# Performance work log

Measured on AMD Instinct MI355X. Metric: run time of the kernel, lower is better.

## Reference

```python
import jax, jax.numpy as jnp
import numpy as np
from jax import lax

STEPS = 200
LR = 0.01
BATCH = 16384
PROJ = 8
HID = 64


def setup_inputs() -> dict:
    key = jax.random.key(0)
    k_spec, k_w1, k_w2, k_r = jax.random.split(key, 4)
    spectrum = jax.random.normal(k_spec, (BATCH, 40), dtype=jnp.float32)
    # forward_model params: MLP 6 -> 64 (tanh) -> 40
    W1 = jax.random.normal(k_w1, (6, HID), dtype=jnp.float32) * 0.3
    b1 = jnp.zeros((HID,), dtype=jnp.float32)
    W2 = jax.random.normal(k_w2, (HID, 40), dtype=jnp.float32) * 0.3
    b2 = jnp.zeros((40,), dtype=jnp.float32)
    # random projection, row-normalized (as in __init__)
    R = jax.random.normal(k_r, (PROJ, 40), dtype=jnp.float32)
    R = R / jnp.linalg.norm(R, axis=1, keepdims=True)
    return {"spectrum": spectrum, "W1": W1, "b1": b1, "W2": W2, "b2": b2, "R": R}


def reference(spectrum, W1, b1, W2, b2, R):
    def fwd_model(u):  # (6,) -> (40,)
        return jnp.tanh(u @ W1 + b1) @ W2 + b2

    def solve(spec):  # spec: (40,) -> u: (6,)
        def step(u, _):
            g_pred = fwd_model(u)
            error = g_pred - spec               # (40,)
            z = R @ error                       # (PROJ,)
            grad_est = R.T @ z                  # (40,)
            u = u - LR * grad_est[:6]
            u = jnp.clip(u, 0.0, 1.0)           # clamp=True
            return u, None

        u0 = jnp.full((6,), 0.5, dtype=spec.dtype)
        u_final, _ = lax.scan(step, u0, None, length=STEPS)
        return u_final

    return jax.vmap(solve)(spectrum)  # (BATCH, 6)
```

## Files before the change

kernel.cpp:

```cpp
#include <hip/hip_runtime.h>


static constexpr float LR_ = 0.01f;

typedef float v2f __attribute__((ext_vector_type(2)));

__device__ __forceinline__ void pin2(v2f& x) { asm volatile("" : "+v"(x)); }

__global__ __launch_bounds__(256)
__attribute__((amdgpu_waves_per_eu(2, 2)))
void solve_k(
    const float* __restrict__ spec, const float* __restrict__ W1,
    const float* __restrict__ b1,   const float* __restrict__ W2,
    const float* __restrict__ b2,   const float* __restrict__ R,
    float* __restrict__ out, int batch)
{
    __shared__ float sQs[64 * 7];
    __shared__ float sSs[240];

    const int t = threadIdx.x;

    if (t < 64) {
        float M[8];
        #pragma unroll
        for (int p = 0; p < 8; ++p) {
            float acc = 0.f;
            for (int k = 0; k < 40; ++k) acc = fmaf(W2[t*40+k], R[p*40+k], acc);
            M[p] = acc;
        }
        #pragma unroll
        for (int j = 0; j < 6; ++j) {
            float acc = 0.f;
            #pragma unroll
            for (int p = 0; p < 8; ++p) acc = fmaf(M[p], R[p*40+j], acc);
            sQs[t*7+j] = -LR_ * acc;
        }
    } else {
        for (int idx = t - 64; idx < 240; idx += 192) {
            int j = idx / 40, k = idx % 40;
            float acc = 0.f;
            #pragma unroll
            for (int p = 0; p < 8; ++p) acc = fmaf(R[p*40+j], R[p*40+k], acc);
            sSs[idx] = -LR_ * acc;
        }
    }
    __syncthreads();

    const int tid = blockIdx.x * 256 + t;
    const int s   = tid >> 3;
    const int sub = tid & 7;
    const int ib  = sub * 8;
    const bool live = (s < batch);
    const int sl = live ? s : 0;

    const float K = 2.8853900817779268f;

    v2f w1kp[6][4], b1kp[4];
    #pragma unroll
    for (int j = 0; j < 6; ++j)
        #pragma unroll
        for (int ip = 0; ip < 4; ++ip) {
            w1kp[j][ip].x = K * W1[j*64 + ib + 2*ip];
            w1kp[j][ip].y = K * W1[j*64 + ib + 2*ip + 1];
        }
    #pragma unroll
    for (int ip = 0; ip < 4; ++ip) {
        b1kp[ip].x = K * b1[ib + 2*ip];
        b1kp[ip].y = K * b1[ib + 2*ip + 1];
    }

    v2f qs2p[8][3];
    float qc[6];
    #pragma unroll
    for (int j = 0; j < 6; ++j) qc[j] = 0.f;
    #pragma unroll
    for (int i = 0; i < 8; ++i)
        #pragma unroll
        for (int m = 0; m < 3; ++m) {
            float a = sQs[(ib + i)*7 + 2*m];
            float b = sQs[(ib + i)*7 + 2*m + 1];
            qs2p[i][m].x = -2.f * a;
            qs2p[i][m].y = -2.f * b;
            qc[2*m]   += a;
            qc[2*m+1] += b;
        }

    float es[6];
    #pragma unroll
    for (int j = 0; j < 6; ++j) es[j] = 0.f;
    const float* sp = spec + sl * 40;
    for (int k = 0; k < 40; ++k) {
        float v = b2[k] - sp[k];
        #pragma unroll
        for (int j = 0; j < 6; ++j) es[j] = fmaf(v, sSs[j*40+k], es[j]);
    }
    v2f c2[3];
    #pragma unroll
    for (int m = 0; m < 3; ++m) {
        c2[m].x = es[2*m]   * 0.125f + qc[2*m];
        c2[m].y = es[2*m+1] * 0.125f + qc[2*m+1];
    }

    #pragma unroll
    for (int j = 0; j < 6; ++j)
        #pragma unroll
        for (int ip = 0; ip < 4; ++ip) pin2(w1kp[j][ip]);
    #pragma unroll
    for (int ip = 0; ip < 4; ++ip) pin2(b1kp[ip]);
    #pragma unroll
    for (int i = 0; i < 8; ++i)
        #pragma unroll
        for (int m = 0; m < 3; ++m) pin2(qs2p[i][m]);
    #pragma unroll
    for (int m = 0; m < 3; ++m) pin2(c2[m]);

    float u[6];
    #pragma unroll
    for (int j = 0; j < 6; ++j) u[j] = 0.5f;

    for (int step = 0; step < 200; ++step) {
        float r[8];
        #pragma unroll
        for (int ip = 0; ip < 4; ++ip) {
            v2f tt = b1kp[ip];
            #pragma unroll
            for (int j = 0; j < 6; ++j) {
                v2f ub = {u[j], u[j]};
                tt = __builtin_elementwise_fma(ub, w1kp[j][ip], tt);
            }
            v2f e1;
            e1.x = __builtin_amdgcn_exp2f(tt.x);
            e1.y = __builtin_amdgcn_exp2f(tt.y);
            e1 += (v2f){1.f, 1.f};
            float rab = __builtin_amdgcn_rcpf(e1.x * e1.y);
            r[2*ip]   = e1.y * rab;
            r[2*ip+1] = e1.x * rab;
        }
        v2f g2[3];
        #pragma unroll
        for (int m = 0; m < 3; ++m) {
            v2f up = {u[2*m], u[2*m+1]};
            g2[m] = __builtin_elementwise_fma(up, (v2f){0.125f, 0.125f}, c2[m]);
        }
        #pragma unroll
        for (int i = 0; i < 8; ++i) {
            v2f hb = {r[i], r[i]};
            #pragma unroll
            for (int m = 0; m < 3; ++m)
                g2[m] = __builtin_elementwise_fma(hb, qs2p[i][m], g2[m]);
        }
        float a0 = g2[0].x, a1 = g2[0].y, a2 = g2[1].x,
              a3 = g2[1].y, a4 = g2[2].x, a5 = g2[2].y;
        asm("s_nop 1\n\t"
            "v_add_f32_dpp %0, %0, %0 quad_perm:[1,0,3,2] row_mask:0xf bank_mask:0xf bound_ctrl:0\n\t"
            "v_add_f32_dpp %1, %1, %1 quad_perm:[1,0,3,2] row_mask:0xf bank_mask:0xf bound_ctrl:0\n\t"
            "v_add_f32_dpp %2, %2, %2 quad_perm:[1,0,3,2] row_mask:0xf bank_mask:0xf bound_ctrl:0\n\t"
            "v_add_f32_dpp %3, %3, %3 quad_perm:[1,0,3,2] row_mask:0xf bank_mask:0xf bound_ctrl:0\n\t"
            "v_add_f32_dpp %4, %4, %4 quad_perm:[1,0,3,2] row_mask:0xf bank_mask:0xf bound_ctrl:0\n\t"
            "v_add_f32_dpp %5, %5, %5 quad_perm:[1,0,3,2] row_mask:0xf bank_mask:0xf bound_ctrl:0\n\t"
            "v_add_f32_dpp %0, %0, %0 quad_perm:[2,3,0,1] row_mask:0xf bank_mask:0xf bound_ctrl:0\n\t"
            "v_add_f32_dpp %1, %1, %1 quad_perm:[2,3,0,1] row_mask:0xf bank_mask:0xf bound_ctrl:0\n\t"
            "v_add_f32_dpp %2, %2, %2 quad_perm:[2,3,0,1] row_mask:0xf bank_mask:0xf bound_ctrl:0\n\t"
            "v_add_f32_dpp %3, %3, %3 quad_perm:[2,3,0,1] row_mask:0xf bank_mask:0xf bound_ctrl:0\n\t"
            "v_add_f32_dpp %4, %4, %4 quad_perm:[2,3,0,1] row_mask:0xf bank_mask:0xf bound_ctrl:0\n\t"
            "v_add_f32_dpp %5, %5, %5 quad_perm:[2,3,0,1] row_mask:0xf bank_mask:0xf bound_ctrl:0\n\t"
            "v_add_f32_dpp %0, %0, %0 row_half_mirror row_mask:0xf bank_mask:0xf bound_ctrl:0\n\t"
            "v_add_f32_dpp %1, %1, %1 row_half_mirror row_mask:0xf bank_mask:0xf bound_ctrl:0\n\t"
            "v_add_f32_dpp %2, %2, %2 row_half_mirror row_mask:0xf bank_mask:0xf bound_ctrl:0\n\t"
            "v_add_f32_dpp %3, %3, %3 row_half_mirror row_mask:0xf bank_mask:0xf bound_ctrl:0\n\t"
            "v_add_f32_dpp %4, %4, %4 row_half_mirror row_mask:0xf bank_mask:0xf bound_ctrl:0\n\t"
            "v_add_f32_dpp %5, %5, %5 row_half_mirror row_mask:0xf bank_mask:0xf bound_ctrl:0\n\t"
            : "+v"(a0), "+v"(a1), "+v"(a2), "+v"(a3), "+v"(a4), "+v"(a5));
        u[0] = __builtin_amdgcn_fmed3f(a0, 0.f, 1.f);
        u[1] = __builtin_amdgcn_fmed3f(a1, 0.f, 1.f);
        u[2] = __builtin_amdgcn_fmed3f(a2, 0.f, 1.f);
        u[3] = __builtin_amdgcn_fmed3f(a3, 0.f, 1.f);
        u[4] = __builtin_amdgcn_fmed3f(a4, 0.f, 1.f);
        u[5] = __builtin_amdgcn_fmed3f(a5, 0.f, 1.f);
    }

    if (live && sub == 0) {
        float* o = out + s * 6;
        #pragma unroll
        for (int j = 0; j < 6; ++j) o[j] = u[j];
    }
}

extern "C" void kernel_launch(void* const* d_in, const int* in_sizes, int n_in,
                              void* d_out, int out_size, void* d_ws, size_t ws_size,
                              hipStream_t stream)
{
    const float* spec = (const float*)d_in[0];
    const float* W1   = (const float*)d_in[1];
    const float* b1   = (const float*)d_in[2];
    const float* W2   = (const float*)d_in[3];
    const float* b2   = (const float*)d_in[4];
    const float* R    = (const float*)d_in[5];
    int batch = in_sizes[0] / 40;

    int threads = batch * 8;
    int blocks  = (threads + 255) / 256;
    hipLaunchKernelGGL(solve_k, dim3(blocks), dim3(256), 0, stream,
                       spec, W1, b1, W2, b2, R, (float*)d_out, batch);
}
```

Baseline: 156.0 us.

## Split each sample across 4 lanes with op_sel packed FMAs

Each sample's 64 hidden units are now split across 4 lanes instead of 8, so every lane holds 16 units in registers. The cross-lane reduction drops from three DPP stages to two. The hidden-layer and output accumulations use inline v_pk_fma_f32 with op_sel to broadcast u and r lanes without building splat vectors, and the output accumulation is split into two independent chains. The sigmoid now uses a separate rcp per element instead of the shared-reciprocal trick. Occupancy is lowered to 1 wave per EU to fit the larger register set, and half as many threads are launched, which trades latency hiding for fewer reduction and broadcast instructions.

```diff
diff --git a/kernel.cpp b/kernel.cpp
--- a/kernel.cpp
+++ b/kernel.cpp
@@ -7,8 +7,21 @@
 
 __device__ __forceinline__ void pin2(v2f& x) { asm volatile("" : "+v"(x)); }
 
+#define PK_FMA_LO(T, U, W)                                                   \
+    asm("v_pk_fma_f32 %0, %1, %2, %0 op_sel:[0,0,0] op_sel_hi:[0,1,1]"       \
+        : "+v"(T) : "v"(U), "v"(W))
+#define PK_FMA_HI(T, U, W)                                                   \
+    asm("v_pk_fma_f32 %0, %1, %2, %0 op_sel:[1,0,0] op_sel_hi:[1,1,1]"       \
+        : "+v"(T) : "v"(U), "v"(W))
+#define PK_MUL_LO(D, U, W)                                                   \
+    asm("v_pk_mul_f32 %0, %1, %2 op_sel:[0,0] op_sel_hi:[0,1]"               \
+        : "=v"(D) : "v"(U), "v"(W))
+#define PK_MUL_HI(D, U, W)                                                   \
+    asm("v_pk_mul_f32 %0, %1, %2 op_sel:[1,0] op_sel_hi:[1,1]"               \
+        : "=v"(D) : "v"(U), "v"(W))
+
 __global__ __launch_bounds__(256)
-__attribute__((amdgpu_waves_per_eu(2, 2)))
+__attribute__((amdgpu_waves_per_eu(1, 1)))
 void solve_k(
     const float* __restrict__ spec, const float* __restrict__ W1,
     const float* __restrict__ b1,   const float* __restrict__ W2,
@@ -47,34 +60,34 @@
     __syncthreads();
 
     const int tid = blockIdx.x * 256 + t;
-    const int s   = tid >> 3;
-    const int sub = tid & 7;
-    const int ib  = sub * 8;
+    const int s   = tid >> 2;
+    const int sub = tid & 3;
+    const int ib  = sub * 16;
     const bool live = (s < batch);
     const int sl = live ? s : 0;
 
     const float K = 2.8853900817779268f;
 
-    v2f w1kp[6][4], b1kp[4];
+    v2f w1kp[6][8], b1kp[8];
     #pragma unroll
     for (int j = 0; j < 6; ++j)
         #pragma unroll
-        for (int ip = 0; ip < 4; ++ip) {
-            w1kp[j][ip].x = K * W1[j*64 + ib + 2*ip];
-            w1kp[j][ip].y = K * W1[j*64 + ib + 2*ip + 1];
-        }
-    #pragma unroll
-    for (int ip = 0; ip < 4; ++ip) {
-        b1kp[ip].x = K * b1[ib + 2*ip];
-        b1kp[ip].y = K * b1[ib + 2*ip + 1];
-    }
-
-    v2f qs2p[8][3];
+        for (int p = 0; p < 8; ++p) {
+            w1kp[j][p].x = K * W1[j*64 + ib + 2*p];
+            w1kp[j][p].y = K * W1[j*64 + ib + 2*p + 1];
+        }
+    #pragma unroll
+    for (int p = 0; p < 8; ++p) {
+        b1kp[p].x = K * b1[ib + 2*p];
+        b1kp[p].y = K * b1[ib + 2*p + 1];
+    }
+
+    v2f qs2p[16][3];
     float qc[6];
     #pragma unroll
     for (int j = 0; j < 6; ++j) qc[j] = 0.f;
     #pragma unroll
-    for (int i = 0; i < 8; ++i)
+    for (int i = 0; i < 16; ++i)
         #pragma unroll
         for (int m = 0; m < 3; ++m) {
             float a = sQs[(ib + i)*7 + 2*m];
@@ -97,60 +110,77 @@
     v2f c2[3];
     #pragma unroll
     for (int m = 0; m < 3; ++m) {
-        c2[m].x = es[2*m]   * 0.125f + qc[2*m];
-        c2[m].y = es[2*m+1] * 0.125f + qc[2*m+1];
-    }
+        c2[m].x = es[2*m]   * 0.25f + qc[2*m];
+        c2[m].y = es[2*m+1] * 0.25f + qc[2*m+1];
+    }
+
+    v2f quarter = {0.25f, 0.25f};
 
     #pragma unroll
     for (int j = 0; j < 6; ++j)
         #pragma unroll
-        for (int ip = 0; ip < 4; ++ip) pin2(w1kp[j][ip]);
-    #pragma unroll
-    for (int ip = 0; ip < 4; ++ip) pin2(b1kp[ip]);
-    #pragma unroll
-    for (int i = 0; i < 8; ++i)
+        for (int p = 0; p < 8; ++p) pin2(w1kp[j][p]);
+    #pragma unroll
+    for (int p = 0; p < 8; ++p) pin2(b1kp[p]);
+    #pragma unroll
+    for (int i = 0; i < 16; ++i)
         #pragma unroll
         for (int m = 0; m < 3; ++m) pin2(qs2p[i][m]);
     #pragma unroll
     for (int m = 0; m < 3; ++m) pin2(c2[m]);
-
-    float u[6];
-    #pragma unroll
-    for (int j = 0; j < 6; ++j) u[j] = 0.5f;
+    pin2(quarter);
+
+    v2f u2[3];
+    #pragma unroll
+    for (int m = 0; m < 3; ++m) u2[m] = (v2f){0.5f, 0.5f};
 
     for (int step = 0; step < 200; ++step) {
-        float r[8];
-        #pragma unroll
-        for (int ip = 0; ip < 4; ++ip) {
-            v2f tt = b1kp[ip];
-            #pragma unroll
-            for (int j = 0; j < 6; ++j) {
-                v2f ub = {u[j], u[j]};
-                tt = __builtin_elementwise_fma(ub, w1kp[j][ip], tt);
+        v2f tt[8];
+        #pragma unroll
+        for (int p = 0; p < 8; ++p) tt[p] = b1kp[p];
+        #pragma unroll
+        for (int jp = 0; jp < 3; ++jp) {
+            #pragma unroll
+            for (int p = 0; p < 8; ++p) { PK_FMA_LO(tt[p], u2[jp], w1kp[2*jp][p]); }
+            #pragma unroll
+            for (int p = 0; p < 8; ++p) { PK_FMA_HI(tt[p], u2[jp], w1kp[2*jp+1][p]); }
+        }
+        v2f r2[8];
+        #pragma unroll
+        for (int p = 0; p < 8; ++p) {
+            v2f e;
+            e.x = __builtin_amdgcn_exp2f(tt[p].x);
+            e.y = __builtin_amdgcn_exp2f(tt[p].y);
+            e += (v2f){1.f, 1.f};
+            r2[p].x = __builtin_amdgcn_rcpf(e.x);
+            r2[p].y = __builtin_amdgcn_rcpf(e.y);
+        }
+        v2f gA0, gA1, gA2, gB0, gB1, gB2;
+        gA0 = __builtin_elementwise_fma(u2[0], quarter, c2[0]);
+        gA1 = __builtin_elementwise_fma(u2[1], quarter, c2[1]);
+        gA2 = __builtin_elementwise_fma(u2[2], quarter, c2[2]);
+        PK_MUL_LO(gB0, r2[4], qs2p[8][0]);
+        PK_MUL_LO(gB1, r2[4], qs2p[8][1]);
+        PK_MUL_LO(gB2, r2[4], qs2p[8][2]);
+        #pragma unroll
+        for (int p = 0; p < 4; ++p) {
+            PK_FMA_LO(gA0, r2[p], qs2p[2*p][0]);
+            PK_FMA_LO(gA1, r2[p], qs2p[2*p][1]);
+            PK_FMA_LO(gA2, r2[p], qs2p[2*p][2]);
+            PK_FMA_HI(gB0, r2[p+4], qs2p[2*p+9 - (p==0 ? 0 : 0)][0]);
+            PK_FMA_HI(gB1, r2[p+4], qs2p[2*p+9][1]);
+            PK_FMA_HI(gB2, r2[p+4], qs2p[2*p+9][2]);
+            PK_FMA_HI(gA0, r2[p], qs2p[2*p+1][0]);
+            PK_FMA_HI(gA1, r2[p], qs2p[2*p+1][1]);
+            PK_FMA_HI(gA2, r2[p], qs2p[2*p+1][2]);
+            if (p < 3) {
+                PK_FMA_LO(gB0, r2[p+5], qs2p[2*p+10][0]);
+                PK_FMA_LO(gB1, r2[p+5], qs2p[2*p+10][1]);
+                PK_FMA_LO(gB2, r2[p+5], qs2p[2*p+10][2]);
             }
-            v2f e1;
-            e1.x = __builtin_amdgcn_exp2f(tt.x);
-            e1.y = __builtin_amdgcn_exp2f(tt.y);
-            e1 += (v2f){1.f, 1.f};
-            float rab = __builtin_amdgcn_rcpf(e1.x * e1.y);
-            r[2*ip]   = e1.y * rab;
-            r[2*ip+1] = e1.x * rab;
-        }
-        v2f g2[3];
-        #pragma unroll
-        for (int m = 0; m < 3; ++m) {
-            v2f up = {u[2*m], u[2*m+1]};
-            g2[m] = __builtin_elementwise_fma(up, (v2f){0.125f, 0.125f}, c2[m]);
-        }
-        #pragma unroll
-        for (int i = 0; i < 8; ++i) {
-            v2f hb = {r[i], r[i]};
-            #pragma unroll
-            for (int m = 0; m < 3; ++m)
-                g2[m] = __builtin_elementwise_fma(hb, qs2p[i][m], g2[m]);
-        }
-        float a0 = g2[0].x, a1 = g2[0].y, a2 = g2[1].x,
-              a3 = g2[1].y, a4 = g2[2].x, a5 = g2[2].y;
+        }
+        v2f h0 = gA0 + gB0, h1 = gA1 + gB1, h2 = gA2 + gB2;
+        float a0 = h0.x, a1 = h0.y, a2 = h1.x, a3 = h1.y, a4 = h2.x, a5 = h2.y;
         asm("s_nop 1\n\t"
             "v_add_f32_dpp %0, %0, %0 quad_perm:[1,0,3,2] row_mask:0xf bank_mask:0xf bound_ctrl:0\n\t"
             "v_add_f32_dpp %1, %1, %1 quad_perm:[1,0,3,2] row_mask:0xf bank_mask:0xf bound_ctrl:0\n\t"
@@ -164,25 +194,20 @@
             "v_add_f32_dpp %3, %3, %3 quad_perm:[2,3,0,1] row_mask:0xf bank_mask:0xf bound_ctrl:0\n\t"
             "v_add_f32_dpp %4, %4, %4 quad_perm:[2,3,0,1] row_mask:0xf bank_mask:0xf bound_ctrl:0\n\t"
             "v_add_f32_dpp %5, %5, %5 quad_perm:[2,3,0,1] row_mask:0xf bank_mask:0xf bound_ctrl:0\n\t"
-            "v_add_f32_dpp %0, %0, %0 row_half_mirror row_mask:0xf bank_mask:0xf bound_ctrl:0\n\t"
-            "v_add_f32_dpp %1, %1, %1 row_half_mirror row_mask:0xf bank_mask:0xf bound_ctrl:0\n\t"
-            "v_add_f32_dpp %2, %2, %2 row_half_mirror row_mask:0xf bank_mask:0xf bound_ctrl:0\n\t"
-            "v_add_f32_dpp %3, %3, %3 row_half_mirror row_mask:0xf bank_mask:0xf bound_ctrl:0\n\t"
-            "v_add_f32_dpp %4, %4, %4 row_half_mirror row_mask:0xf bank_mask:0xf bound_ctrl:0\n\t"
-            "v_add_f32_dpp %5, %5, %5 row_half_mirror row_mask:0xf bank_mask:0xf bound_ctrl:0\n\t"
             : "+v"(a0), "+v"(a1), "+v"(a2), "+v"(a3), "+v"(a4), "+v"(a5));
-        u[0] = __builtin_amdgcn_fmed3f(a0, 0.f, 1.f);
-        u[1] = __builtin_amdgcn_fmed3f(a1, 0.f, 1.f);
-        u[2] = __builtin_amdgcn_fmed3f(a2, 0.f, 1.f);
-        u[3] = __builtin_amdgcn_fmed3f(a3, 0.f, 1.f);
-        u[4] = __builtin_amdgcn_fmed3f(a4, 0.f, 1.f);
-        u[5] = __builtin_amdgcn_fmed3f(a5, 0.f, 1.f);
+        u2[0].x = __builtin_amdgcn_fmed3f(a0, 0.f, 1.f);
+        u2[0].y = __builtin_amdgcn_fmed3f(a1, 0.f, 1.f);
+        u2[1].x = __builtin_amdgcn_fmed3f(a2, 0.f, 1.f);
+        u2[1].y = __builtin_amdgcn_fmed3f(a3, 0.f, 1.f);
+        u2[2].x = __builtin_amdgcn_fmed3f(a4, 0.f, 1.f);
+        u2[2].y = __builtin_amdgcn_fmed3f(a5, 0.f, 1.f);
     }
 
     if (live && sub == 0) {
         float* o = out + s * 6;
-        #pragma unroll
-        for (int j = 0; j < 6; ++j) o[j] = u[j];
+        o[0] = u2[0].x; o[1] = u2[0].y;
+        o[2] = u2[1].x; o[3] = u2[1].y;
+        o[4] = u2[2].x; o[5] = u2[2].y;
     }
 }
 
@@ -198,7 +223,7 @@
     const float* R    = (const float*)d_in[5];
     int batch = in_sizes[0] / 40;
 
-    int threads = batch * 8;
+    int threads = batch * 4;
     int blocks  = (threads + 255) / 256;
     hipLaunchKernelGGL(solve_k, dim3(blocks), dim3(256), 0, stream,
                        spec, W1, b1, W2, b2, R, (float*)d_out, batch);
```

Result: faster. 144.2 us (-7.5%).

## Process two samples per lane with inline packed FMAs, halving thread count

Applied to the files above, without the earlier changes.

Each 8-lane group now solves two samples at once (A and B), so the register-resident W1 and Q weights are reused across two independent chains and the launch uses half the threads. Packed-FMA inline asm with op_sel broadcasts u and r lanes without building splat vectors. The output accumulation is split into two partial sums to shorten the dependency chain. The sigmoid now uses one reciprocal per element instead of a shared reciprocal. Waves per EU drop to 1, trading occupancy for more instruction-level parallelism and registers.

```diff
diff --git a/kernel.cpp b/kernel.cpp
--- a/kernel.cpp
+++ b/kernel.cpp
@@ -7,8 +7,18 @@
 
 __device__ __forceinline__ void pin2(v2f& x) { asm volatile("" : "+v"(x)); }
 
+#define PK_FMA_LO(T, U, W)                                                   \
+    asm("v_pk_fma_f32 %0, %1, %2, %0 op_sel:[0,0,0] op_sel_hi:[0,1,1]"       \
+        : "+v"(T) : "v"(U), "v"(W))
+#define PK_FMA_HI(T, U, W)                                                   \
+    asm("v_pk_fma_f32 %0, %1, %2, %0 op_sel:[1,0,0] op_sel_hi:[1,1,1]"       \
+        : "+v"(T) : "v"(U), "v"(W))
+#define PK_MUL_LO(D, U, W)                                                   \
+    asm("v_pk_mul_f32 %0, %1, %2 op_sel:[0,0] op_sel_hi:[0,1]"               \
+        : "=v"(D) : "v"(U), "v"(W))
+
 __global__ __launch_bounds__(256)
-__attribute__((amdgpu_waves_per_eu(2, 2)))
+__attribute__((amdgpu_waves_per_eu(1, 1)))
 void solve_k(
     const float* __restrict__ spec, const float* __restrict__ W1,
     const float* __restrict__ b1,   const float* __restrict__ W2,
@@ -46,12 +56,16 @@
     }
     __syncthreads();
 
-    const int tid = blockIdx.x * 256 + t;
-    const int s   = tid >> 3;
-    const int sub = tid & 7;
+    const int l   = t & 63;
+    const int w   = t >> 6;
+    const int sub = l & 7;
     const int ib  = sub * 8;
-    const bool live = (s < batch);
-    const int sl = live ? s : 0;
+    const int grp = l >> 3;
+    const int wid = blockIdx.x * 4 + w;
+    const int sA  = wid * 16 + grp;
+    const int sB  = wid * 16 + 8 + grp;
+    const bool liveA = (sA < batch), liveB = (sB < batch);
+    const int slA = liveA ? sA : 0, slB = liveB ? sB : 0;
 
     const float K = 2.8853900817779268f;
 
@@ -59,14 +73,14 @@
     #pragma unroll
     for (int j = 0; j < 6; ++j)
         #pragma unroll
-        for (int ip = 0; ip < 4; ++ip) {
-            w1kp[j][ip].x = K * W1[j*64 + ib + 2*ip];
-            w1kp[j][ip].y = K * W1[j*64 + ib + 2*ip + 1];
-        }
-    #pragma unroll
-    for (int ip = 0; ip < 4; ++ip) {
-        b1kp[ip].x = K * b1[ib + 2*ip];
-        b1kp[ip].y = K * b1[ib + 2*ip + 1];
+        for (int p = 0; p < 4; ++p) {
+            w1kp[j][p].x = K * W1[j*64 + ib + 2*p];
+            w1kp[j][p].y = K * W1[j*64 + ib + 2*p + 1];
+        }
+    #pragma unroll
+    for (int p = 0; p < 4; ++p) {
+        b1kp[p].x = K * b1[ib + 2*p];
+        b1kp[p].y = K * b1[ib + 2*p + 1];
     }
 
     v2f qs2p[8][3];
@@ -85,72 +99,141 @@
             qc[2*m+1] += b;
         }
 
-    float es[6];
-    #pragma unroll
-    for (int j = 0; j < 6; ++j) es[j] = 0.f;
-    const float* sp = spec + sl * 40;
+    float esA[6], esB[6];
+    #pragma unroll
+    for (int j = 0; j < 6; ++j) { esA[j] = 0.f; esB[j] = 0.f; }
+    const float* spA = spec + slA * 40;
+    const float* spB = spec + slB * 40;
     for (int k = 0; k < 40; ++k) {
-        float v = b2[k] - sp[k];
-        #pragma unroll
-        for (int j = 0; j < 6; ++j) es[j] = fmaf(v, sSs[j*40+k], es[j]);
-    }
-    v2f c2[3];
+        float vA = b2[k] - spA[k];
+        float vB = b2[k] - spB[k];
+        #pragma unroll
+        for (int j = 0; j < 6; ++j) {
+            esA[j] = fmaf(vA, sSs[j*40+k], esA[j]);
+            esB[j] = fmaf(vB, sSs[j*40+k], esB[j]);
+        }
+    }
+    v2f c2A[3], c2B[3];
     #pragma unroll
     for (int m = 0; m < 3; ++m) {
-        c2[m].x = es[2*m]   * 0.125f + qc[2*m];
-        c2[m].y = es[2*m+1] * 0.125f + qc[2*m+1];
-    }
+        c2A[m].x = esA[2*m]   * 0.125f + qc[2*m];
+        c2A[m].y = esA[2*m+1] * 0.125f + qc[2*m+1];
+        c2B[m].x = esB[2*m]   * 0.125f + qc[2*m];
+        c2B[m].y = esB[2*m+1] * 0.125f + qc[2*m+1];
+    }
+
+    v2f eighth = {0.125f, 0.125f};
 
     #pragma unroll
     for (int j = 0; j < 6; ++j)
         #pragma unroll
-        for (int ip = 0; ip < 4; ++ip) pin2(w1kp[j][ip]);
-    #pragma unroll
-    for (int ip = 0; ip < 4; ++ip) pin2(b1kp[ip]);
+        for (int p = 0; p < 4; ++p) pin2(w1kp[j][p]);
+    #pragma unroll
+    for (int p = 0; p < 4; ++p) pin2(b1kp[p]);
     #pragma unroll
     for (int i = 0; i < 8; ++i)
         #pragma unroll
         for (int m = 0; m < 3; ++m) pin2(qs2p[i][m]);
     #pragma unroll
-    for (int m = 0; m < 3; ++m) pin2(c2[m]);
-
-    float u[6];
-    #pragma unroll
-    for (int j = 0; j < 6; ++j) u[j] = 0.5f;
+    for (int m = 0; m < 3; ++m) { pin2(c2A[m]); pin2(c2B[m]); }
+    pin2(eighth);
+
+    v2f u2A[3], u2B[3];
+    #pragma unroll
+    for (int m = 0; m < 3; ++m) { u2A[m] = (v2f){0.5f, 0.5f}; u2B[m] = (v2f){0.5f, 0.5f}; }
 
     for (int step = 0; step < 200; ++step) {
-        float r[8];
-        #pragma unroll
-        for (int ip = 0; ip < 4; ++ip) {
-            v2f tt = b1kp[ip];
-            #pragma unroll
-            for (int j = 0; j < 6; ++j) {
-                v2f ub = {u[j], u[j]};
-                tt = __builtin_elementwise_fma(ub, w1kp[j][ip], tt);
-            }
-            v2f e1;
-            e1.x = __builtin_amdgcn_exp2f(tt.x);
-            e1.y = __builtin_amdgcn_exp2f(tt.y);
-            e1 += (v2f){1.f, 1.f};
-            float rab = __builtin_amdgcn_rcpf(e1.x * e1.y);
-            r[2*ip]   = e1.y * rab;
-            r[2*ip+1] = e1.x * rab;
-        }
-        v2f g2[3];
-        #pragma unroll
-        for (int m = 0; m < 3; ++m) {
-            v2f up = {u[2*m], u[2*m+1]};
-            g2[m] = __builtin_elementwise_fma(up, (v2f){0.125f, 0.125f}, c2[m]);
-        }
-        #pragma unroll
-        for (int i = 0; i < 8; ++i) {
-            v2f hb = {r[i], r[i]};
-            #pragma unroll
-            for (int m = 0; m < 3; ++m)
-                g2[m] = __builtin_elementwise_fma(hb, qs2p[i][m], g2[m]);
-        }
-        float a0 = g2[0].x, a1 = g2[0].y, a2 = g2[1].x,
-              a3 = g2[1].y, a4 = g2[2].x, a5 = g2[2].y;
+        v2f ttA[4], ttB[4];
+        #pragma unroll
+        for (int p = 0; p < 4; ++p) { ttA[p] = b1kp[p]; ttB[p] = b1kp[p]; }
+        #pragma unroll
+        for (int jp = 0; jp < 3; ++jp) {
+            #pragma unroll
+            for (int p = 0; p < 4; ++p) { PK_FMA_LO(ttA[p], u2A[jp], w1kp[2*jp][p]); }
+            #pragma unroll
+            for (int p = 0; p < 4; ++p) { PK_FMA_LO(ttB[p], u2B[jp], w1kp[2*jp][p]); }
+            #pragma unroll
+            for (int p = 0; p < 4; ++p) { PK_FMA_HI(ttA[p], u2A[jp], w1kp[2*jp+1][p]); }
+            #pragma unroll
+            for (int p = 0; p < 4; ++p) { PK_FMA_HI(ttB[p], u2B[jp], w1kp[2*jp+1][p]); }
+        }
+        v2f rA[4], rB[4];
+        #pragma unroll
+        for (int p = 0; p < 4; ++p) {
+            v2f eA, eB;
+            eA.x = __builtin_amdgcn_exp2f(ttA[p].x);
+            eA.y = __builtin_amdgcn_exp2f(ttA[p].y);
+            eB.x = __builtin_amdgcn_exp2f(ttB[p].x);
+            eB.y = __builtin_amdgcn_exp2f(ttB[p].y);
+            eA += (v2f){1.f, 1.f};
+            eB += (v2f){1.f, 1.f};
+            rA[p].x = __builtin_amdgcn_rcpf(eA.x);
+            rA[p].y = __builtin_amdgcn_rcpf(eA.y);
+            rB[p].x = __builtin_amdgcn_rcpf(eB.x);
+            rB[p].y = __builtin_amdgcn_rcpf(eB.y);
+        }
+        v2f gXA0, gXA1, gXA2, gYA0, gYA1, gYA2;
+        v2f gXB0, gXB1, gXB2, gYB0, gYB1, gYB2;
+        gXA0 = __builtin_elementwise_fma(u2A[0], eighth, c2A[0]);
+        gXA1 = __builtin_elementwise_fma(u2A[1], eighth, c2A[1]);
+        gXA2 = __builtin_elementwise_fma(u2A[2], eighth, c2A[2]);
+        gXB0 = __builtin_elementwise_fma(u2B[0], eighth, c2B[0]);
+        gXB1 = __builtin_elementwise_fma(u2B[1], eighth, c2B[1]);
+        gXB2 = __builtin_elementwise_fma(u2B[2], eighth, c2B[2]);
+        PK_MUL_LO(gYA0, rA[2], qs2p[4][0]);
+        PK_MUL_LO(gYA1, rA[2], qs2p[4][1]);
+        PK_MUL_LO(gYA2, rA[2], qs2p[4][2]);
+        PK_MUL_LO(gYB0, rB[2], qs2p[4][0]);
+        PK_MUL_LO(gYB1, rB[2], qs2p[4][1]);
+        PK_MUL_LO(gYB2, rB[2], qs2p[4][2]);
+        PK_FMA_LO(gXA0, rA[0], qs2p[0][0]);
+        PK_FMA_LO(gXA1, rA[0], qs2p[0][1]);
+        PK_FMA_LO(gXA2, rA[0], qs2p[0][2]);
+        PK_FMA_LO(gXB0, rB[0], qs2p[0][0]);
+        PK_FMA_LO(gXB1, rB[0], qs2p[0][1]);
+        PK_FMA_LO(gXB2, rB[0], qs2p[0][2]);
+        PK_FMA_HI(gYA0, rA[2], qs2p[5][0]);
+        PK_FMA_HI(gYA1, rA[2], qs2p[5][1]);
+        PK_FMA_HI(gYA2, rA[2], qs2p[5][2]);
+        PK_FMA_HI(gYB0, rB[2], qs2p[5][0]);
+        PK_FMA_HI(gYB1, rB[2], qs2p[5][1]);
+        PK_FMA_HI(gYB2, rB[2], qs2p[5][2]);
+        PK_FMA_HI(gXA0, rA[0], qs2p[1][0]);
+        PK_FMA_HI(gXA1, rA[0], qs2p[1][1]);
+        PK_FMA_HI(gXA2, rA[0], qs2p[1][2]);
+        PK_FMA_HI(gXB0, rB[0], qs2p[1][0]);
+        PK_FMA_HI(gXB1, rB[0], qs2p[1][1]);
+        PK_FMA_HI(gXB2, rB[0], qs2p[1][2]);
+        PK_FMA_LO(gYA0, rA[3], qs2p[6][0]);
+        PK_FMA_LO(gYA1, rA[3], qs2p[6][1]);
+        PK_FMA_LO(gYA2, rA[3], qs2p[6][2]);
+        PK_FMA_LO(gYB0, rB[3], qs2p[6][0]);
+        PK_FMA_LO(gYB1, rB[3], qs2p[6][1]);
+        PK_FMA_LO(gYB2, rB[3], qs2p[6][2]);
+        PK_FMA_LO(gXA0, rA[1], qs2p[2][0]);
+        PK_FMA_LO(gXA1, rA[1], qs2p[2][1]);
+        PK_FMA_LO(gXA2, rA[1], qs2p[2][2]);
+        PK_FMA_LO(gXB0, rB[1], qs2p[2][0]);
+        PK_FMA_LO(gXB1, rB[1], qs2p[2][1]);
+        PK_FMA_LO(gXB2, rB[1], qs2p[2][2]);
+        PK_FMA_HI(gYA0, rA[3], qs2p[7][0]);
+        PK_FMA_HI(gYA1, rA[3], qs2p[7][1]);
+        PK_FMA_HI(gYA2, rA[3], qs2p[7][2]);
+        PK_FMA_HI(gYB0, rB[3], qs2p[7][0]);
+        PK_FMA_HI(gYB1, rB[3], qs2p[7][1]);
+        PK_FMA_HI(gYB2, rB[3], qs2p[7][2]);
+        PK_FMA_HI(gXA0, rA[1], qs2p[3][0]);
+        PK_FMA_HI(gXA1, rA[1], qs2p[3][1]);
+        PK_FMA_HI(gXA2, rA[1], qs2p[3][2]);
+        PK_FMA_HI(gXB0, rB[1], qs2p[3][0]);
+        PK_FMA_HI(gXB1, rB[1], qs2p[3][1]);
+        PK_FMA_HI(gXB2, rB[1], qs2p[3][2]);
+        v2f hA0 = gXA0 + gYA0, hA1 = gXA1 + gYA1, hA2 = gXA2 + gYA2;
+        v2f hB0 = gXB0 + gYB0, hB1 = gXB1 + gYB1, hB2 = gXB2 + gYB2;
+        float aA0 = hA0.x, aA1 = hA0.y, aA2 = hA1.x,
+              aA3 = hA1.y, aA4 = hA2.x, aA5 = hA2.y;
+        float aB0 = hB0.x, aB1 = hB0.y, aB2 = hB1.x,
+              aB3 = hB1.y, aB4 = hB2.x, aB5 = hB2.y;
         asm("s_nop 1\n\t"
             "v_add_f32_dpp %0, %0, %0 quad_perm:[1,0,3,2] row_mask:0xf bank_mask:0xf bound_ctrl:0\n\t"
             "v_add_f32_dpp %1, %1, %1 quad_perm:[1,0,3,2] row_mask:0xf bank_mask:0xf bound_ctrl:0\n\t"
@@ -158,31 +241,65 @@
             "v_add_f32_dpp %3, %3, %3 quad_perm:[1,0,3,2] row_mask:0xf bank_mask:0xf bound_ctrl:0\n\t"
             "v_add_f32_dpp %4, %4, %4 quad_perm:[1,0,3,2] row_mask:0xf bank_mask:0xf bound_ctrl:0\n\t"
             "v_add_f32_dpp %5, %5, %5 quad_perm:[1,0,3,2] row_mask:0xf bank_mask:0xf bound_ctrl:0\n\t"
+            "v_add_f32_dpp %6, %6, %6 quad_perm:[1,0,3,2] row_mask:0xf bank_mask:0xf bound_ctrl:0\n\t"
+            "v_add_f32_dpp %7, %7, %7 quad_perm:[1,0,3,2] row_mask:0xf bank_mask:0xf bound_ctrl:0\n\t"
+            "v_add_f32_dpp %8, %8, %8 quad_perm:[1,0,3,2] row_mask:0xf bank_mask:0xf bound_ctrl:0\n\t"
+            "v_add_f32_dpp %9, %9, %9 quad_perm:[1,0,3,2] row_mask:0xf bank_mask:0xf bound_ctrl:0\n\t"
+            "v_add_f32_dpp %10, %10, %10 quad_perm:[1,0,3,2] row_mask:0xf bank_mask:0xf bound_ctrl:0\n\t"
+            "v_add_f32_dpp %11, %11, %11 quad_perm:[1,0,3,2] row_mask:0xf bank_mask:0xf bound_ctrl:0\n\t"
             "v_add_f32_dpp %0, %0, %0 quad_perm:[2,3,0,1] row_mask:0xf bank_mask:0xf bound_ctrl:0\n\t"
             "v_add_f32_dpp %1, %1, %1 quad_perm:[2,3,0,1] row_mask:0xf bank_mask:0xf bound_ctrl:0\n\t"
             "v_add_f32_dpp %2, %2, %2 quad_perm:[2,3,0,1] row_mask:0xf bank_mask:0xf bound_ctrl:0\n\t"
             "v_add_f32_dpp %3, %3, %3 quad_perm:[2,3,0,1] row_mask:0xf bank_mask:0xf bound_ctrl:0\n\t"
             "v_add_f32_dpp %4, %4, %4 quad_perm:[2,3,0,1] row_mask:0xf bank_mask:0xf bound_ctrl:0\n\t"
             "v_add_f32_dpp %5, %5, %5 quad_perm:[2,3,0,1] row_mask:0xf bank_mask:0xf bound_ctrl:0\n\t"
+            "v_add_f32_dpp %6, %6, %6 quad_perm:[2,3,0,1] row_mask:0xf bank_mask:0xf bound_ctrl:0\n\t"
+            "v_add_f32_dpp %7, %7, %7 quad_perm:[2,3,0,1] row_mask:0xf bank_mask:0xf bound_ctrl:0\n\t"
+            "v_add_f32_dpp %8, %8, %8 quad_perm:[2,3,0,1] row_mask:0xf bank_mask:0xf bound_ctrl:0\n\t"
+            "v_add_f32_dpp %9, %9, %9 quad_perm:[2,3,0,1] row_mask:0xf bank_mask:0xf bound_ctrl:0\n\t"
+            "v_add_f32_dpp %10, %10, %10 quad_perm:[2,3,0,1] row_mask:0xf bank_mask:0xf bound_ctrl:0\n\t"
+            "v_add_f32_dpp %11, %11, %11 quad_perm:[2,3,0,1] row_mask:0xf bank_mask:0xf bound_ctrl:0\n\t"
             "v_add_f32_dpp %0, %0, %0 row_half_mirror row_mask:0xf bank_mask:0xf bound_ctrl:0\n\t"
             "v_add_f32_dpp %1, %1, %1 row_half_mirror row_mask:0xf bank_mask:0xf bound_ctrl:0\n\t"
             "v_add_f32_dpp %2, %2, %2 row_half_mirror row_mask:0xf bank_mask:0xf bound_ctrl:0\n\t"
             "v_add_f32_dpp %3, %3, %3 row_half_mirror row_mask:0xf bank_mask:0xf bound_ctrl:0\n\t"
             "v_add_f32_dpp %4, %4, %4 row_half_mirror row_mask:0xf bank_mask:0xf bound_ctrl:0\n\t"
             "v_add_f32_dpp %5, %5, %5 row_half_mirror row_mask:0xf bank_mask:0xf bound_ctrl:0\n\t"
-            : "+v"(a0), "+v"(a1), "+v"(a2), "+v"(a3), "+v"(a4), "+v"(a5));
-        u[0] = __builtin_amdgcn_fmed3f(a0, 0.f, 1.f);
-        u[1] = __builtin_amdgcn_fmed3f(a1, 0.f, 1.f);
-        u[2] = __builtin_amdgcn_fmed3f(a2, 0.f, 1.f);
-        u[3] = __builtin_amdgcn_fmed3f(a3, 0.f, 1.f);
-        u[4] = __builtin_amdgcn_fmed3f(a4, 0.f, 1.f);
-        u[5] = __builtin_amdgcn_fmed3f(a5, 0.f, 1.f);
-    }
-
-    if (live && sub == 0) {
-        float* o = out + s * 6;
-        #pragma unroll
-        for (int j = 0; j < 6; ++j) o[j] = u[j];
+            "v_add_f32_dpp %6, %6, %6 row_half_mirror row_mask:0xf bank_mask:0xf bound_ctrl:0\n\t"
+            "v_add_f32_dpp %7, %7, %7 row_half_mirror row_mask:0xf bank_mask:0xf bound_ctrl:0\n\t"
+            "v_add_f32_dpp %8, %8, %8 row_half_mirror row_mask:0xf bank_mask:0xf bound_ctrl:0\n\t"
+            "v_add_f32_dpp %9, %9, %9 row_half_mirror row_mask:0xf bank_mask:0xf bound_ctrl:0\n\t"
+            "v_add_f32_dpp %10, %10, %10 row_half_mirror row_mask:0xf bank_mask:0xf bound_ctrl:0\n\t"
+            "v_add_f32_dpp %11, %11, %11 row_half_mirror row_mask:0xf bank_mask:0xf bound_ctrl:0\n\t"
+            : "+v"(aA0), "+v"(aA1), "+v"(aA2), "+v"(aA3), "+v"(aA4), "+v"(aA5),
+              "+v"(aB0), "+v"(aB1), "+v"(aB2), "+v"(aB3), "+v"(aB4), "+v"(aB5));
+        u2A[0].x = __builtin_amdgcn_fmed3f(aA0, 0.f, 1.f);
+        u2A[0].y = __builtin_amdgcn_fmed3f(aA1, 0.f, 1.f);
+        u2A[1].x = __builtin_amdgcn_fmed3f(aA2, 0.f, 1.f);
+        u2A[1].y = __builtin_amdgcn_fmed3f(aA3, 0.f, 1.f);
+        u2A[2].x = __builtin_amdgcn_fmed3f(aA4, 0.f, 1.f);
+        u2A[2].y = __builtin_amdgcn_fmed3f(aA5, 0.f, 1.f);
+        u2B[0].x = __builtin_amdgcn_fmed3f(aB0, 0.f, 1.f);
+        u2B[0].y = __builtin_amdgcn_fmed3f(aB1, 0.f, 1.f);
+        u2B[1].x = __builtin_amdgcn_fmed3f(aB2, 0.f, 1.f);
+        u2B[1].y = __builtin_amdgcn_fmed3f(aB3, 0.f, 1.f);
+        u2B[2].x = __builtin_amdgcn_fmed3f(aB4, 0.f, 1.f);
+        u2B[2].y = __builtin_amdgcn_fmed3f(aB5, 0.f, 1.f);
+    }
+
+    if (sub == 0) {
+        if (liveA) {
+            float* o = out + sA * 6;
+            o[0] = u2A[0].x; o[1] = u2A[0].y;
+            o[2] = u2A[1].x; o[3] = u2A[1].y;
+            o[4] = u2A[2].x; o[5] = u2A[2].y;
+        }
+        if (liveB) {
+            float* o = out + sB * 6;
+            o[0] = u2B[0].x; o[1] = u2B[0].y;
+            o[2] = u2B[1].x; o[3] = u2B[1].y;
+            o[4] = u2B[2].x; o[5] = u2B[2].y;
+        }
     }
 }
 
@@ -198,7 +315,7 @@
     const float* R    = (const float*)d_in[5];
     int batch = in_sizes[0] / 40;
 
-    int threads = batch * 8;
+    int threads = batch * 4;
     int blocks  = (threads + 255) / 256;
     hipLaunchKernelGGL(solve_k, dim3(blocks), dim3(256), 0, stream,
                        spec, W1, b1, W2, b2, R, (float*)d_out, batch);
```

New measurement: 161.1 us. 3.3% more time.
